# Kernel optimization log

Hardware: AMD Instinct MI355X
Metric: run time of the kernel (lower is better)

Reference implementation:

```python
import jax, jax.numpy as jnp
import numpy as np

BLOCK_SIZE = 32
QMAX = 31.0   # 6-bit symmetric: representable range [-32, 31], scale by absmax/31
QMIN = -32.0


def axs6_dequant(w: jnp.ndarray, block_size: int = BLOCK_SIZE) -> jnp.ndarray:
    """Block-wise 6-bit symmetric fake-quantization (quantize + dequantize)."""
    shape = w.shape
    wf = w.reshape(-1, block_size)                       # [n_blocks, block]
    scale = jnp.max(jnp.abs(wf), axis=1, keepdims=True) / QMAX
    scale = jnp.where(scale == 0, jnp.ones_like(scale), scale)
    q = jnp.clip(jnp.round(wf / scale), QMIN, QMAX)
    return (q * scale).reshape(shape)


def setup_inputs() -> dict:
    key = jax.random.key(0)
    k_x, k_w, k_b = jax.random.split(key, 3)
    C_in, C_out, K = 256, 512, 3
    x = jax.random.normal(k_x, (32, C_in, 56, 56), dtype=jnp.float32)
    # kaiming_uniform_(a=sqrt(5)) -> bound = sqrt(6 / ((1 + 5) * fan_in)) = 1/sqrt(fan_in)
    fan_in = C_in * K * K
    bound = 1.0 / np.sqrt(fan_in)
    weight = jax.random.uniform(k_w, (C_out, C_in, K, K), dtype=jnp.float32,
                                minval=-bound, maxval=bound)
    bias = jax.random.uniform(k_b, (C_out,), dtype=jnp.float32,
                              minval=-bound, maxval=bound)
    return {"x": x, "weight": weight, "bias": bias}


def reference(x, weight, bias):
    w_dq = axs6_dequant(weight, BLOCK_SIZE)
    out = jax.lax.conv_general_dilated(
        x, w_dq,
        window_strides=(1, 1),
        padding=((1, 1), (1, 1)),
        rhs_dilation=(1, 1),
        feature_group_count=1,
        dimension_numbers=("NCHW", "OIHW", "NCHW"),
    )
    return out + bias[None, :, None, None]
```

## Files before the change

kernel.cpp:

```cpp
#include <hip/hip_runtime.h>
#include <hip/hip_bf16.h>

typedef __bf16 bf16_t;
typedef __attribute__((ext_vector_type(8))) __bf16 bf16x8;
typedef __attribute__((ext_vector_type(4))) float f32x4;

#define C_IN   256
#define C_OUT  512
#define HW     3136
#define NB     32
#define HP     58
#define NQBLK  36864

#define BM   256
#define BN   224
#define BPIX 352
#define NWG  896

typedef const __attribute__((address_space(1))) unsigned int gu32;
typedef __attribute__((address_space(3))) unsigned int lu32;
__device__ __forceinline__ void gl16(const void* g, void* l) {
    __builtin_amdgcn_global_load_lds((gu32*)g, (lu32*)l, 16, 0, 0);
}
#define BAR()    __builtin_amdgcn_s_barrier()
#define PRIO(x)  __builtin_amdgcn_s_setprio(x)
#define SCHED0() __builtin_amdgcn_sched_barrier(0)

__global__ void k_dequant(const float* __restrict__ w, bf16_t* __restrict__ wt) {
    int b = blockIdx.x * blockDim.x + threadIdx.x;
    if (b >= NQBLK) return;
    const float* src = w + (size_t)b * 32;
    float v[32];
    float amax = 0.f;
    #pragma unroll
    for (int i = 0; i < 32; i += 4) {
        float4 t = *reinterpret_cast<const float4*>(src + i);
        v[i] = t.x; v[i+1] = t.y; v[i+2] = t.z; v[i+3] = t.w;
        amax = fmaxf(amax, fmaxf(fmaxf(fabsf(t.x), fabsf(t.y)),
                                 fmaxf(fabsf(t.z), fabsf(t.w))));
    }
    float scale = amax / 31.0f;
    if (scale == 0.f) scale = 1.f;
    #pragma unroll
    for (int i = 0; i < 32; i++) {
        float q = rintf(v[i] / scale);
        q = fminf(31.f, fmaxf(-32.f, q));
        float dq = q * scale;
        int flat = b * 32 + i;
        int p    = flat % 9;
        int rest = flat / 9;
        int ci   = rest & 255;
        int co   = rest >> 8;
        wt[((size_t)(p * C_OUT + co) << 8) + ci] = (bf16_t)dq;
    }
}

__global__ void k_halo_zero(bf16_t* __restrict__ xT) {
    int idx = blockIdx.x * 256 + threadIdx.x;
    if (idx >= NB * 228 * 32) return;
    int c8 = idx & 31;
    int t  = idx >> 5;
    int p  = t % 228;
    int n  = t / 228;
    int hh, ww;
    if      (p < 58)  { hh = 0;           ww = p; }
    else if (p < 116) { hh = 57;          ww = p - 58; }
    else if (p < 172) { hh = p - 116 + 1; ww = 0; }
    else              { hh = p - 172 + 1; ww = 57; }
    size_t e = (((size_t)n * HP + hh) * HP + ww) * C_IN + c8 * 8;
    *reinterpret_cast<uint4*>(xT + e) = make_uint4(0, 0, 0, 0);
}

__global__ void k_x_nhwc(const float* __restrict__ x, bf16_t* __restrict__ xT) {
    __shared__ float tile[64][65];
    const int n   = blockIdx.z;
    const int cb  = blockIdx.y * 64;
    const int hwb = blockIdx.x * 64;
    const int t   = threadIdx.x;

    const int col = t & 63;
    const int r0  = t >> 6;
    #pragma unroll
    for (int k = 0; k < 16; k++) {
        int r = r0 * 16 + k;
        tile[r][col] = x[((size_t)(n * C_IN + cb + r)) * HW + hwb + col];
    }
    __syncthreads();

    const int j  = t >> 2;
    const int co = (t & 3) * 16;
    const int hw = hwb + j;
    const int hh = hw / 56, ww = hw - hh * 56;
    __align__(16) bf16_t vals[16];
    #pragma unroll
    for (int k = 0; k < 16; k++)
        vals[k] = (bf16_t)tile[co + k][j];
    bf16_t* dst = xT + (((size_t)n * HP + hh + 1) * HP + (ww + 1)) * C_IN + cb + co;
    *reinterpret_cast<uint4*>(dst)     = *reinterpret_cast<uint4*>(&vals[0]);
    *reinterpret_cast<uint4*>(dst + 8) = *reinterpret_cast<uint4*>(&vals[8]);
}

__global__ __launch_bounds__(512, 2) void k_conv_gemm(
    const bf16_t* __restrict__ xT, const bf16_t* __restrict__ wt,
    const float* __restrict__ bias, float* __restrict__ out)
{
    __shared__ __align__(16) bf16_t As[2][BM][64];
    __shared__ __align__(16) bf16_t Bs[2][BPIX][64];

    const int tid  = threadIdx.x;
    const int lane = tid & 63;
    const int wid  = tid >> 6;
    const int wr   = wid >> 1;
    const int wc   = wid & 1;

    const int orig  = blockIdx.x;
    const int wgid  = (orig & 7) * 112 + (orig >> 3);
    const int co0   = (wgid & 1) * BM;
    const int sband = wgid >> 1;
    const int nimg  = sband / 14;
    const int R0    = (sband - nimg * 14) * 4;

    const int prow = tid >> 3;
    const int lcx  = (tid & 7) ^ (prow & 7);

    const bf16_t* pAsrc = wt + ((size_t)(co0 + prow) << 8) + lcx * 8;
    const bf16_t* pBsrc = xT + ((size_t)(nimg * HP + R0) * HP + prow) * C_IN + lcx * 8;

    auto stageA = [&](int buf, int c, int p) {
        const bf16_t* src = pAsrc + ((size_t)p << 17) + (c << 6);
        bf16_t* dst = &As[buf][wid * 8][0];
        #pragma unroll
        for (int i = 0; i < 4; i++)
            gl16(src + (i << 14), dst + i * 4096);
    };
    auto stageB = [&](int buf, int c) {
        const bf16_t* src = pBsrc + (c << 6);
        bf16_t* dst = &Bs[buf][wid * 8][0];
        #pragma unroll
        for (int i = 0; i < 5; i++)
            gl16(src + i * 16384, dst + i * 4096);
        if (tid < 224)
            gl16(src + 5 * 16384, dst + 5 * 4096);
    };

    const int rl = lane & 15;
    const int kg = lane >> 4;

    int a_off[4][2];
    #pragma unroll
    for (int m = 0; m < 4; m++) {
        int row = wr * 64 + m * 16 + rl;
        a_off[m][0] = row * 64 + ((kg       ^ (rl & 7)) * 8);
        a_off[m][1] = row * 64 + (((4 + kg) ^ (rl & 7)) * 8);
    }
    int base_pix[7];
    #pragma unroll
    for (int j = 0; j < 7; j++) {
        int nn = wc * 112 + j * 16 + rl;
        int br = nn / 56, bc = nn - br * 56;
        base_pix[j] = (br + 1) * 58 + bc + 1;
    }

    f32x4 acc[4][7];
    #pragma unroll
    for (int m = 0; m < 4; m++)
        #pragma unroll
        for (int j = 0; j < 7; j++)
            acc[m][j] = f32x4{0.f, 0.f, 0.f, 0.f};

    stageB(0, 0);
    stageA(0, 0, 0);
    asm volatile("s_waitcnt vmcnt(0)" ::: "memory");
    BAR();
    SCHED0();

    bf16x8 aF[4][2], bF[7][2];

    #pragma unroll 1
    for (int c = 0; c < 4; ++c) {
        const int cb = c & 1;
        #pragma unroll 1
        for (int p = 0; p < 9; ++p) {
            const int t    = c * 9 + p;
            const int tpar = t & 1;

            if (t + 1 < 36) {
                int pn = (p == 8) ? 0 : p + 1;
                int cn = (p == 8) ? c + 1 : c;
                stageA(tpar ^ 1, cn, pn);
            }
            if (p == 1 && c < 3)
                stageB(cb ^ 1, c + 1);

            const int q3 = p / 3;
            const int sh = (q3 - 1) * 58 + (p - q3 * 3) - 1;

            const bf16_t* abase = &As[tpar][0][0];
            #pragma unroll
            for (int m = 0; m < 4; m++) {
                aF[m][0] = *reinterpret_cast<const bf16x8*>(abase + a_off[m][0]);
                aF[m][1] = *reinterpret_cast<const bf16x8*>(abase + a_off[m][1]);
            }
            const bf16_t* bbase = &Bs[cb][0][0];
            #pragma unroll
            for (int j = 0; j < 7; j++) {
                int pix = base_pix[j] + sh;
                const bf16_t* rp = bbase + pix * 64;
                int key = (pix & 7);
                bF[j][0] = *reinterpret_cast<const bf16x8*>(rp + ((kg       ^ key) * 8));
                bF[j][1] = *reinterpret_cast<const bf16x8*>(rp + (((4 + kg) ^ key) * 8));
            }

            PRIO(1);
            #pragma unroll
            for (int m = 0; m < 4; m++)
                #pragma unroll
                for (int j = 0; j < 7; j++) {
                    acc[m][j] = __builtin_amdgcn_mfma_f32_16x16x32_bf16(aF[m][0], bF[j][0], acc[m][j], 0, 0, 0);
                    acc[m][j] = __builtin_amdgcn_mfma_f32_16x16x32_bf16(aF[m][1], bF[j][1], acc[m][j], 0, 0, 0);
                }
            PRIO(0);

            asm volatile("s_waitcnt vmcnt(0)" ::: "memory");
            BAR();
            SCHED0();
        }
    }

    int hw_off[7];
    #pragma unroll
    for (int j = 0; j < 7; j++) {
        int nn = wc * 112 + j * 16 + rl;
        int br = nn / 56, bc = nn - br * 56;
        hw_off[j] = (R0 + br) * 56 + bc;
    }
    const size_t obase = (size_t)nimg * C_OUT * HW;
    #pragma unroll
    for (int m = 0; m < 4; m++) {
        int cob = co0 + wr * 64 + m * 16 + ((lane >> 4) << 2);
        #pragma unroll
        for (int i = 0; i < 4; i++) {
            int co = cob + i;
            float bv = bias[co];
            float* orow = out + obase + (size_t)co * HW;
            #pragma unroll
            for (int j = 0; j < 7; j++)
                orow[hw_off[j]] = acc[m][j][i] + bv;
        }
    }
}

extern "C" void kernel_launch(void* const* d_in, const int* in_sizes, int n_in,
                              void* d_out, int out_size, void* d_ws, size_t ws_size,
                              hipStream_t stream) {
    const float* x    = (const float*)d_in[0];
    const float* w    = (const float*)d_in[1];
    const float* bias = (const float*)d_in[2];
    float* out = (float*)d_out;

    bf16_t* xT = (bf16_t*)d_ws;
    bf16_t* wt = (bf16_t*)((char*)d_ws + (size_t)NB * HP * HP * C_IN * 2);

    k_halo_zero<<<dim3((NB * 228 * 32 + 255) / 256), dim3(256), 0, stream>>>(xT);
    k_x_nhwc<<<dim3(49, 4, NB), dim3(256), 0, stream>>>(x, xT);
    k_dequant<<<dim3((NQBLK + 255) / 256), dim3(256), 0, stream>>>(w, wt);
    k_conv_gemm<<<dim3(NWG), dim3(512), 0, stream>>>(xT, wt, bias, out);
}
```

Before: 314.7 us.

## Halve K-tile to 32 and add a triple-buffered A pipeline with split B staging

Shrinks the per-step reduction chunk from 64 to 32 channels, which halves LDS per buffer and doubles the number of main-loop iterations. The weight tile becomes triple-buffered with a two-step prefetch, and the waitcnt is relaxed to vmcnt(2) so one load stays in flight across the barrier. The input-band staging is split into three parts spread over iterations. The aim is to overlap global loads with MFMA work and raise occupancy, at the cost of twice as many barriers and a smaller MFMA batch per barrier.

```diff
diff --git a/kernel.cpp b/kernel.cpp
--- a/kernel.cpp
+++ b/kernel.cpp
@@ -12,9 +12,7 @@
 #define HP     58
 #define NQBLK  36864
 
-#define BM   256
-#define BN   224
-#define BPIX 352
+#define BK   32
 #define NWG  896
 
 typedef const __attribute__((address_space(1))) unsigned int gu32;
@@ -104,8 +102,8 @@
     const bf16_t* __restrict__ xT, const bf16_t* __restrict__ wt,
     const float* __restrict__ bias, float* __restrict__ out)
 {
-    __shared__ __align__(16) bf16_t As[2][BM][64];
-    __shared__ __align__(16) bf16_t Bs[2][BPIX][64];
+    __shared__ __align__(16) bf16_t As[3][256][BK];
+    __shared__ __align__(16) bf16_t Bs[2][384][BK];
 
     const int tid  = threadIdx.x;
     const int lane = tid & 63;
@@ -115,50 +113,43 @@
 
     const int orig  = blockIdx.x;
     const int wgid  = (orig & 7) * 112 + (orig >> 3);
-    const int co0   = (wgid & 1) * BM;
+    const int co0   = (wgid & 1) * 256;
     const int sband = wgid >> 1;
     const int nimg  = sband / 14;
     const int R0    = (sband - nimg * 14) * 4;
 
-    const int prow = tid >> 3;
-    const int lcx  = (tid & 7) ^ (prow & 7);
-
-    const bf16_t* pAsrc = wt + ((size_t)(co0 + prow) << 8) + lcx * 8;
-    const bf16_t* pBsrc = xT + ((size_t)(nimg * HP + R0) * HP + prow) * C_IN + lcx * 8;
-
-    auto stageA = [&](int buf, int c, int p) {
-        const bf16_t* src = pAsrc + ((size_t)p << 17) + (c << 6);
-        bf16_t* dst = &As[buf][wid * 8][0];
-        #pragma unroll
-        for (int i = 0; i < 4; i++)
-            gl16(src + (i << 14), dst + i * 4096);
+    const int trow = tid >> 2;
+    const int lcx  = (tid & 3) ^ ((trow ^ (trow >> 2)) & 3);
+    const bf16_t* pAsrc = wt + ((size_t)(co0 + trow) << 8) + lcx * 8;
+    const size_t bandStart = (size_t)(nimg * HP + R0) * HP;
+    const bf16_t* pBsrc = xT + (bandStart + trow) * C_IN + lcx * 8;
+
+    auto stageA = [&](int slot, int cn, int pn) {
+        const bf16_t* src = pAsrc + ((size_t)pn << 17) + (cn << 5);
+        bf16_t* dst = &As[slot][0][0] + wid * 512;
+        gl16(src, dst);
+        gl16(src + (128 << 8), dst + 4096);
     };
-    auto stageB = [&](int buf, int c) {
-        const bf16_t* src = pBsrc + (c << 6);
-        bf16_t* dst = &Bs[buf][wid * 8][0];
-        #pragma unroll
-        for (int i = 0; i < 5; i++)
-            gl16(src + i * 16384, dst + i * 4096);
-        if (tid < 224)
-            gl16(src + 5 * 16384, dst + 5 * 4096);
+    auto stageBpart = [&](int buf, int cn, int part) {
+        const bf16_t* src = pBsrc + ((size_t)part << 15) + (cn << 5);
+        bf16_t* dst = &Bs[buf][0][0] + part * 4096 + wid * 512;
+        gl16(src, dst);
     };
 
     const int rl = lane & 15;
     const int kg = lane >> 4;
-
-    int a_off[4][2];
+    int a_off[4];
     #pragma unroll
     for (int m = 0; m < 4; m++) {
         int row = wr * 64 + m * 16 + rl;
-        a_off[m][0] = row * 64 + ((kg       ^ (rl & 7)) * 8);
-        a_off[m][1] = row * 64 + (((4 + kg) ^ (rl & 7)) * 8);
-    }
-    int base_pix[7];
+        a_off[m] = row * BK + ((kg ^ ((row ^ (row >> 2)) & 3)) * 8);
+    }
+    int bpix[7];
     #pragma unroll
     for (int j = 0; j < 7; j++) {
         int nn = wc * 112 + j * 16 + rl;
         int br = nn / 56, bc = nn - br * 56;
-        base_pix[j] = (br + 1) * 58 + bc + 1;
+        bpix[j] = (br + 1) * 58 + bc + 1;
     }
 
     f32x4 acc[4][7];
@@ -168,62 +159,61 @@
         for (int j = 0; j < 7; j++)
             acc[m][j] = f32x4{0.f, 0.f, 0.f, 0.f};
 
-    stageB(0, 0);
+    stageBpart(0, 0, 0); stageBpart(0, 0, 1); stageBpart(0, 0, 2);
     stageA(0, 0, 0);
-    asm volatile("s_waitcnt vmcnt(0)" ::: "memory");
+    stageA(1, 0, 1);
+    asm volatile("s_waitcnt vmcnt(2)" ::: "memory");
     BAR();
     SCHED0();
 
-    bf16x8 aF[4][2], bF[7][2];
+    bf16x8 aF[4], bF[7];
+    int sr = 0;
 
     #pragma unroll 1
-    for (int c = 0; c < 4; ++c) {
-        const int cb = c & 1;
+    for (int c = 0; c < 8; ++c) {
+        const int bb = c & 1;
         #pragma unroll 1
         for (int p = 0; p < 9; ++p) {
-            const int t    = c * 9 + p;
-            const int tpar = t & 1;
-
-            if (t + 1 < 36) {
-                int pn = (p == 8) ? 0 : p + 1;
-                int cn = (p == 8) ? c + 1 : c;
-                stageA(tpar ^ 1, cn, pn);
+            const int t = c * 9 + p;
+
+            if (t < 70) {
+                int pn = p + 2, cn = c;
+                if (pn >= 9) { pn -= 9; cn++; }
+                int sw = sr + 2; if (sw >= 3) sw -= 3;
+                stageA(sw, cn, pn);
             }
-            if (p == 1 && c < 3)
-                stageB(cb ^ 1, c + 1);
+            if (c < 7 && p >= 1 && p <= 3)
+                stageBpart(bb ^ 1, c + 1, p - 1);
 
             const int q3 = p / 3;
             const int sh = (q3 - 1) * 58 + (p - q3 * 3) - 1;
-
-            const bf16_t* abase = &As[tpar][0][0];
-            #pragma unroll
-            for (int m = 0; m < 4; m++) {
-                aF[m][0] = *reinterpret_cast<const bf16x8*>(abase + a_off[m][0]);
-                aF[m][1] = *reinterpret_cast<const bf16x8*>(abase + a_off[m][1]);
-            }
-            const bf16_t* bbase = &Bs[cb][0][0];
+            const bf16_t* ab = &As[sr][0][0];
+            #pragma unroll
+            for (int m = 0; m < 4; m++)
+                aF[m] = *reinterpret_cast<const bf16x8*>(ab + a_off[m]);
+            const bf16_t* bbp = &Bs[bb][0][0];
             #pragma unroll
             for (int j = 0; j < 7; j++) {
-                int pix = base_pix[j] + sh;
-                const bf16_t* rp = bbase + pix * 64;
-                int key = (pix & 7);
-                bF[j][0] = *reinterpret_cast<const bf16x8*>(rp + ((kg       ^ key) * 8));
-                bF[j][1] = *reinterpret_cast<const bf16x8*>(rp + (((4 + kg) ^ key) * 8));
+                int pix = bpix[j] + sh;
+                int off = pix * BK + ((kg ^ ((pix ^ (pix >> 2)) & 3)) * 8);
+                bF[j] = *reinterpret_cast<const bf16x8*>(bbp + off);
             }
 
             PRIO(1);
             #pragma unroll
             for (int m = 0; m < 4; m++)
                 #pragma unroll
-                for (int j = 0; j < 7; j++) {
-                    acc[m][j] = __builtin_amdgcn_mfma_f32_16x16x32_bf16(aF[m][0], bF[j][0], acc[m][j], 0, 0, 0);
-                    acc[m][j] = __builtin_amdgcn_mfma_f32_16x16x32_bf16(aF[m][1], bF[j][1], acc[m][j], 0, 0, 0);
-                }
+                for (int j = 0; j < 7; j++)
+                    acc[m][j] = __builtin_amdgcn_mfma_f32_16x16x32_bf16(aF[m], bF[j], acc[m][j], 0, 0, 0);
             PRIO(0);
 
-            asm volatile("s_waitcnt vmcnt(0)" ::: "memory");
+            if (t < 70)
+                asm volatile("s_waitcnt vmcnt(2)" ::: "memory");
+            else
+                asm volatile("s_waitcnt vmcnt(0)" ::: "memory");
             BAR();
             SCHED0();
+            sr++; if (sr >= 3) sr -= 3;
         }
     }
 
```

Measured after the change: 361.2 us. +14.8%, slower.

## Stage shifted input tiles per tap and split K-step into four barrier-interleaved phases

Applied to the files above, without the earlier changes.

Replaces the halo-band input tile, which was loaded once per channel chunk and indexed with per-tap pixel shifts, with a per-tap B tile of 224 shifted pixels reloaded every K-step. Each K-step is split into four phases so B and A global-to-LDS loads for the next steps are issued between MFMA groups. A is prefetched two steps ahead and B one step ahead. This aims to overlap loads with MFMA work and shrink LDS footprint, but it reloads input data nine times per channel chunk and adds many more barriers per step.

```diff
diff --git a/kernel.cpp b/kernel.cpp
--- a/kernel.cpp
+++ b/kernel.cpp
@@ -12,9 +12,7 @@
 #define HP     58
 #define NQBLK  36864
 
-#define BM   256
-#define BN   224
-#define BPIX 352
+#define NT   36
 #define NWG  896
 
 typedef const __attribute__((address_space(1))) unsigned int gu32;
@@ -104,8 +102,8 @@
     const bf16_t* __restrict__ xT, const bf16_t* __restrict__ wt,
     const float* __restrict__ bias, float* __restrict__ out)
 {
-    __shared__ __align__(16) bf16_t As[2][BM][64];
-    __shared__ __align__(16) bf16_t Bs[2][BPIX][64];
+    __shared__ __align__(16) bf16_t As[2][256][64];
+    __shared__ __align__(16) bf16_t Bs[2][224][64];
 
     const int tid  = threadIdx.x;
     const int lane = tid & 63;
@@ -115,50 +113,60 @@
 
     const int orig  = blockIdx.x;
     const int wgid  = (orig & 7) * 112 + (orig >> 3);
-    const int co0   = (wgid & 1) * BM;
+    const int co0   = (wgid & 1) * 256;
     const int sband = wgid >> 1;
     const int nimg  = sband / 14;
     const int R0    = (sband - nimg * 14) * 4;
 
-    const int prow = tid >> 3;
-    const int lcx  = (tid & 7) ^ (prow & 7);
-
-    const bf16_t* pAsrc = wt + ((size_t)(co0 + prow) << 8) + lcx * 8;
-    const bf16_t* pBsrc = xT + ((size_t)(nimg * HP + R0) * HP + prow) * C_IN + lcx * 8;
-
-    auto stageA = [&](int buf, int c, int p) {
-        const bf16_t* src = pAsrc + ((size_t)p << 17) + (c << 6);
-        bf16_t* dst = &As[buf][wid * 8][0];
+    const int trow = tid >> 3;
+    const int lcx  = (tid & 7) ^ (trow & 7);
+
+    const bf16_t* pA[4];
+    const bf16_t* pB[4];
+    #pragma unroll
+    for (int i = 0; i < 4; i++) {
+        pA[i] = wt + ((size_t)(co0 + i * 64 + trow) << 8) + lcx * 8;
+        int r  = i * 64 + trow;
+        int br = r / 56, bc = r - br * 56;
+        pB[i] = xT + (((size_t)nimg * HP + R0 + br + 1) * HP + (bc + 1)) * C_IN + lcx * 8;
+    }
+
+    auto stageA = [&](int buf, int tk) {
+        const size_t off = ((size_t)(tk >> 2) << 17) + ((tk & 3) << 6);
+        bf16_t* dst = &As[buf][0][0] + wid * 512;
         #pragma unroll
         for (int i = 0; i < 4; i++)
-            gl16(src + (i << 14), dst + i * 4096);
+            gl16(pA[i] + off, dst + i * 4096);
     };
-    auto stageB = [&](int buf, int c) {
-        const bf16_t* src = pBsrc + (c << 6);
-        bf16_t* dst = &Bs[buf][wid * 8][0];
-        #pragma unroll
-        for (int i = 0; i < 5; i++)
-            gl16(src + i * 16384, dst + i * 4096);
-        if (tid < 224)
-            gl16(src + 5 * 16384, dst + 5 * 4096);
+    auto stageB = [&](int buf, int tk, int half) {
+        const int p  = tk >> 2;
+        const int q3 = p / 3;
+        const int off = ((q3 - 1) * HP + (p - q3 * 3) - 1) * C_IN + ((tk & 3) << 6);
+        bf16_t* dst = &Bs[buf][0][0] + wid * 512;
+        if (half == 0) {
+            gl16(pB[0] + off, dst);
+            gl16(pB[1] + off, dst + 4096);
+        } else {
+            gl16(pB[2] + off, dst + 8192);
+            if (tid < 256)
+                gl16(pB[3] + off, dst + 12288);
+        }
     };
 
     const int rl = lane & 15;
     const int kg = lane >> 4;
-
-    int a_off[4][2];
+    int a_off[4][2], b_off[7][2];
     #pragma unroll
     for (int m = 0; m < 4; m++) {
         int row = wr * 64 + m * 16 + rl;
-        a_off[m][0] = row * 64 + ((kg       ^ (rl & 7)) * 8);
-        a_off[m][1] = row * 64 + (((4 + kg) ^ (rl & 7)) * 8);
-    }
-    int base_pix[7];
+        a_off[m][0] = row * 64 + ((kg       ^ (row & 7)) * 8);
+        a_off[m][1] = row * 64 + (((4 + kg) ^ (row & 7)) * 8);
+    }
     #pragma unroll
     for (int j = 0; j < 7; j++) {
-        int nn = wc * 112 + j * 16 + rl;
-        int br = nn / 56, bc = nn - br * 56;
-        base_pix[j] = (br + 1) * 58 + bc + 1;
+        int row = wc * 112 + j * 16 + rl;
+        b_off[j][0] = row * 64 + ((kg       ^ (row & 7)) * 8);
+        b_off[j][1] = row * 64 + (((4 + kg) ^ (row & 7)) * 8);
     }
 
     f32x4 acc[4][7];
@@ -168,63 +176,104 @@
         for (int j = 0; j < 7; j++)
             acc[m][j] = f32x4{0.f, 0.f, 0.f, 0.f};
 
-    stageB(0, 0);
-    stageA(0, 0, 0);
-    asm volatile("s_waitcnt vmcnt(0)" ::: "memory");
+    stageA(0, 0);
+    stageB(0, 0, 0); stageB(0, 0, 1);
+    stageA(1, 1);
+    asm volatile("s_waitcnt vmcnt(4)" ::: "memory");
     BAR();
     SCHED0();
 
-    bf16x8 aF[4][2], bF[7][2];
+    bf16x8 aF[4][2], bF[2][2];
 
     #pragma unroll 1
-    for (int c = 0; c < 4; ++c) {
-        const int cb = c & 1;
-        #pragma unroll 1
-        for (int p = 0; p < 9; ++p) {
-            const int t    = c * 9 + p;
-            const int tpar = t & 1;
-
-            if (t + 1 < 36) {
-                int pn = (p == 8) ? 0 : p + 1;
-                int cn = (p == 8) ? c + 1 : c;
-                stageA(tpar ^ 1, cn, pn);
+    for (int t = 0; t < NT; ++t) {
+        const int cur = t & 1;
+        const bf16_t* ab = &As[cur][0][0];
+        const bf16_t* bb = &Bs[cur][0][0];
+
+        #pragma unroll
+        for (int m = 0; m < 4; m++) {
+            aF[m][0] = *reinterpret_cast<const bf16x8*>(ab + a_off[m][0]);
+            aF[m][1] = *reinterpret_cast<const bf16x8*>(ab + a_off[m][1]);
+        }
+        #pragma unroll
+        for (int j = 0; j < 2; j++) {
+            bF[j][0] = *reinterpret_cast<const bf16x8*>(bb + b_off[j][0]);
+            bF[j][1] = *reinterpret_cast<const bf16x8*>(bb + b_off[j][1]);
+        }
+        if (t + 1 < NT) stageB(cur ^ 1, t + 1, 0);
+        BAR();
+        asm volatile("s_waitcnt lgkmcnt(0)" ::: "memory");
+        SCHED0();
+        PRIO(1);
+        #pragma unroll
+        for (int m = 0; m < 4; m++)
+            #pragma unroll
+            for (int j = 0; j < 2; j++) {
+                acc[m][j] = __builtin_amdgcn_mfma_f32_16x16x32_bf16(aF[m][0], bF[j][0], acc[m][j], 0, 0, 0);
+                acc[m][j] = __builtin_amdgcn_mfma_f32_16x16x32_bf16(aF[m][1], bF[j][1], acc[m][j], 0, 0, 0);
             }
-            if (p == 1 && c < 3)
-                stageB(cb ^ 1, c + 1);
-
-            const int q3 = p / 3;
-            const int sh = (q3 - 1) * 58 + (p - q3 * 3) - 1;
-
-            const bf16_t* abase = &As[tpar][0][0];
+        PRIO(0);
+        BAR();
+
+        #pragma unroll
+        for (int j = 0; j < 2; j++) {
+            bF[j][0] = *reinterpret_cast<const bf16x8*>(bb + b_off[j + 2][0]);
+            bF[j][1] = *reinterpret_cast<const bf16x8*>(bb + b_off[j + 2][1]);
+        }
+        if (t + 1 < NT) stageB(cur ^ 1, t + 1, 1);
+        BAR();
+        asm volatile("s_waitcnt lgkmcnt(0)" ::: "memory");
+        SCHED0();
+        PRIO(1);
+        #pragma unroll
+        for (int m = 0; m < 4; m++)
             #pragma unroll
-            for (int m = 0; m < 4; m++) {
-                aF[m][0] = *reinterpret_cast<const bf16x8*>(abase + a_off[m][0]);
-                aF[m][1] = *reinterpret_cast<const bf16x8*>(abase + a_off[m][1]);
+            for (int j = 0; j < 2; j++) {
+                acc[m][j + 2] = __builtin_amdgcn_mfma_f32_16x16x32_bf16(aF[m][0], bF[j][0], acc[m][j + 2], 0, 0, 0);
+                acc[m][j + 2] = __builtin_amdgcn_mfma_f32_16x16x32_bf16(aF[m][1], bF[j][1], acc[m][j + 2], 0, 0, 0);
             }
-            const bf16_t* bbase = &Bs[cb][0][0];
+        PRIO(0);
+        BAR();
+
+        #pragma unroll
+        for (int j = 0; j < 2; j++) {
+            bF[j][0] = *reinterpret_cast<const bf16x8*>(bb + b_off[j + 4][0]);
+            bF[j][1] = *reinterpret_cast<const bf16x8*>(bb + b_off[j + 4][1]);
+        }
+        BAR();
+        asm volatile("s_waitcnt lgkmcnt(0)" ::: "memory");
+        SCHED0();
+        PRIO(1);
+        #pragma unroll
+        for (int m = 0; m < 4; m++)
             #pragma unroll
-            for (int j = 0; j < 7; j++) {
-                int pix = base_pix[j] + sh;
-                const bf16_t* rp = bbase + pix * 64;
-                int key = (pix & 7);
-                bF[j][0] = *reinterpret_cast<const bf16x8*>(rp + ((kg       ^ key) * 8));
-                bF[j][1] = *reinterpret_cast<const bf16x8*>(rp + (((4 + kg) ^ key) * 8));
+            for (int j = 0; j < 2; j++) {
+                acc[m][j + 4] = __builtin_amdgcn_mfma_f32_16x16x32_bf16(aF[m][0], bF[j][0], acc[m][j + 4], 0, 0, 0);
+                acc[m][j + 4] = __builtin_amdgcn_mfma_f32_16x16x32_bf16(aF[m][1], bF[j][1], acc[m][j + 4], 0, 0, 0);
             }
-
-            PRIO(1);
-            #pragma unroll
-            for (int m = 0; m < 4; m++)
-                #pragma unroll
-                for (int j = 0; j < 7; j++) {
-                    acc[m][j] = __builtin_amdgcn_mfma_f32_16x16x32_bf16(aF[m][0], bF[j][0], acc[m][j], 0, 0, 0);
-                    acc[m][j] = __builtin_amdgcn_mfma_f32_16x16x32_bf16(aF[m][1], bF[j][1], acc[m][j], 0, 0, 0);
-                }
-            PRIO(0);
-
+        PRIO(0);
+        BAR();
+
+        bF[0][0] = *reinterpret_cast<const bf16x8*>(bb + b_off[6][0]);
+        bF[0][1] = *reinterpret_cast<const bf16x8*>(bb + b_off[6][1]);
+        if (t + 2 < NT) stageA(cur, t + 2);
+        BAR();
+        asm volatile("s_waitcnt lgkmcnt(0)" ::: "memory");
+        SCHED0();
+        PRIO(1);
+        #pragma unroll
+        for (int m = 0; m < 4; m++) {
+            acc[m][6] = __builtin_amdgcn_mfma_f32_16x16x32_bf16(aF[m][0], bF[0][0], acc[m][6], 0, 0, 0);
+            acc[m][6] = __builtin_amdgcn_mfma_f32_16x16x32_bf16(aF[m][1], bF[0][1], acc[m][6], 0, 0, 0);
+        }
+        PRIO(0);
+        if (t + 2 < NT)
+            asm volatile("s_waitcnt vmcnt(4)" ::: "memory");
+        else
             asm volatile("s_waitcnt vmcnt(0)" ::: "memory");
-            BAR();
-            SCHED0();
-        }
+        BAR();
+        SCHED0();
     }
 
     int hw_off[7];
```

After: 316.3 us. No clear change (+0.5%).

## Replace band-tiled conv GEMM with smaller 128x128 implicit-GEMM tiles

Applied to the files above, without the earlier changes.

The conv GEMM moves from 512-thread workgroups with 256-channel by 4-row spatial bands, where the input band is staged once per channel chunk and reused across all nine taps, to 256-thread workgroups computing 128x128 tiles over flattened pixels. Each of the 36 K-steps now restages both the weight tile and a shifted input tile. This drops the per-tap input reuse from the halo band and adds global traffic. In exchange it gets more workgroups, higher occupancy per CU and simpler, uniform staging.

```diff
diff --git a/kernel.cpp b/kernel.cpp
--- a/kernel.cpp
+++ b/kernel.cpp
@@ -12,10 +12,8 @@
 #define HP     58
 #define NQBLK  36864
 
-#define BM   256
-#define BN   224
-#define BPIX 352
-#define NWG  896
+#define NT   36
+#define NWG  3136
 
 typedef const __attribute__((address_space(1))) unsigned int gu32;
 typedef __attribute__((address_space(3))) unsigned int lu32;
@@ -100,12 +98,12 @@
     *reinterpret_cast<uint4*>(dst + 8) = *reinterpret_cast<uint4*>(&vals[8]);
 }
 
-__global__ __launch_bounds__(512, 2) void k_conv_gemm(
+__global__ __launch_bounds__(256, 4) void k_conv_gemm(
     const bf16_t* __restrict__ xT, const bf16_t* __restrict__ wt,
     const float* __restrict__ bias, float* __restrict__ out)
 {
-    __shared__ __align__(16) bf16_t As[2][BM][64];
-    __shared__ __align__(16) bf16_t Bs[2][BPIX][64];
+    __shared__ __align__(16) bf16_t As[2][128][64];
+    __shared__ __align__(16) bf16_t Bs[2][128][64];
 
     const int tid  = threadIdx.x;
     const int lane = tid & 63;
@@ -113,128 +111,122 @@
     const int wr   = wid >> 1;
     const int wc   = wid & 1;
 
-    const int orig  = blockIdx.x;
-    const int wgid  = (orig & 7) * 112 + (orig >> 3);
-    const int co0   = (wgid & 1) * BM;
-    const int sband = wgid >> 1;
-    const int nimg  = sband / 14;
-    const int R0    = (sband - nimg * 14) * 4;
-
-    const int prow = tid >> 3;
-    const int lcx  = (tid & 7) ^ (prow & 7);
-
-    const bf16_t* pAsrc = wt + ((size_t)(co0 + prow) << 8) + lcx * 8;
-    const bf16_t* pBsrc = xT + ((size_t)(nimg * HP + R0) * HP + prow) * C_IN + lcx * 8;
-
-    auto stageA = [&](int buf, int c, int p) {
-        const bf16_t* src = pAsrc + ((size_t)p << 17) + (c << 6);
-        bf16_t* dst = &As[buf][wid * 8][0];
+    const int orig = blockIdx.x;
+    const int wgid = (orig & 7) * 392 + (orig >> 3);
+    const int co0  = (wgid & 3) * 128;
+    const int s0   = (wgid >> 2) * 128;
+
+    const int trow = tid >> 3;
+    const int lcx  = (tid & 7) ^ (trow & 7);
+
+    int aoff[4], boff[4];
+    #pragma unroll
+    for (int i = 0; i < 4; i++) {
+        aoff[i] = ((co0 + i * 32 + trow) << 8) + lcx * 8;
+        int px = s0 + i * 32 + trow;
+        int n  = px / HW;
+        int hw = px - n * HW;
+        int hh = hw / 56, ww = hw - hh * 56;
+        boff[i] = ((n * HP + hh + 1) * HP + ww + 1) * C_IN + lcx * 8;
+    }
+
+    auto stage = [&](int buf, int tk) {
+        const int p  = tk >> 2;
+        const int kc = (tk & 3) << 6;
+        const size_t aT = (size_t)p * (C_OUT << 8) + kc;
+        const int q3 = p / 3;
+        const int bT = ((q3 - 1) * HP + (p - q3 * 3) - 1) * C_IN + kc;
+        bf16_t* dA = &As[buf][0][0] + wid * 512;
+        bf16_t* dB = &Bs[buf][0][0] + wid * 512;
         #pragma unroll
         for (int i = 0; i < 4; i++)
-            gl16(src + (i << 14), dst + i * 4096);
-    };
-    auto stageB = [&](int buf, int c) {
-        const bf16_t* src = pBsrc + (c << 6);
-        bf16_t* dst = &Bs[buf][wid * 8][0];
-        #pragma unroll
-        for (int i = 0; i < 5; i++)
-            gl16(src + i * 16384, dst + i * 4096);
-        if (tid < 224)
-            gl16(src + 5 * 16384, dst + 5 * 4096);
+            gl16(wt + aoff[i] + aT, dA + i * 2048);
+        #pragma unroll
+        for (int i = 0; i < 4; i++)
+            gl16(xT + boff[i] + bT, dB + i * 2048);
     };
 
     const int rl = lane & 15;
     const int kg = lane >> 4;
-
-    int a_off[4][2];
+    int a_off[4][2], b_off[4][2];
     #pragma unroll
     for (int m = 0; m < 4; m++) {
         int row = wr * 64 + m * 16 + rl;
         a_off[m][0] = row * 64 + ((kg       ^ (rl & 7)) * 8);
         a_off[m][1] = row * 64 + (((4 + kg) ^ (rl & 7)) * 8);
     }
-    int base_pix[7];
-    #pragma unroll
-    for (int j = 0; j < 7; j++) {
-        int nn = wc * 112 + j * 16 + rl;
-        int br = nn / 56, bc = nn - br * 56;
-        base_pix[j] = (br + 1) * 58 + bc + 1;
-    }
-
-    f32x4 acc[4][7];
+    #pragma unroll
+    for (int j = 0; j < 4; j++) {
+        int row = wc * 64 + j * 16 + rl;
+        b_off[j][0] = row * 64 + ((kg       ^ (rl & 7)) * 8);
+        b_off[j][1] = row * 64 + (((4 + kg) ^ (rl & 7)) * 8);
+    }
+
+    f32x4 acc[4][4];
     #pragma unroll
     for (int m = 0; m < 4; m++)
         #pragma unroll
-        for (int j = 0; j < 7; j++)
+        for (int j = 0; j < 4; j++)
             acc[m][j] = f32x4{0.f, 0.f, 0.f, 0.f};
 
-    stageB(0, 0);
-    stageA(0, 0, 0);
+    stage(0, 0);
     asm volatile("s_waitcnt vmcnt(0)" ::: "memory");
     BAR();
     SCHED0();
 
-    bf16x8 aF[4][2], bF[7][2];
-
     #pragma unroll 1
-    for (int c = 0; c < 4; ++c) {
-        const int cb = c & 1;
-        #pragma unroll 1
-        for (int p = 0; p < 9; ++p) {
-            const int t    = c * 9 + p;
-            const int tpar = t & 1;
-
-            if (t + 1 < 36) {
-                int pn = (p == 8) ? 0 : p + 1;
-                int cn = (p == 8) ? c + 1 : c;
-                stageA(tpar ^ 1, cn, pn);
-            }
-            if (p == 1 && c < 3)
-                stageB(cb ^ 1, c + 1);
-
-            const int q3 = p / 3;
-            const int sh = (q3 - 1) * 58 + (p - q3 * 3) - 1;
-
-            const bf16_t* abase = &As[tpar][0][0];
-            #pragma unroll
-            for (int m = 0; m < 4; m++) {
-                aF[m][0] = *reinterpret_cast<const bf16x8*>(abase + a_off[m][0]);
-                aF[m][1] = *reinterpret_cast<const bf16x8*>(abase + a_off[m][1]);
-            }
-            const bf16_t* bbase = &Bs[cb][0][0];
-            #pragma unroll
-            for (int j = 0; j < 7; j++) {
-                int pix = base_pix[j] + sh;
-                const bf16_t* rp = bbase + pix * 64;
-                int key = (pix & 7);
-                bF[j][0] = *reinterpret_cast<const bf16x8*>(rp + ((kg       ^ key) * 8));
-                bF[j][1] = *reinterpret_cast<const bf16x8*>(rp + (((4 + kg) ^ key) * 8));
-            }
-
+    for (int t = 0; t < NT; ++t) {
+        const int cur = t & 1;
+        if (t + 1 < NT) stage(cur ^ 1, t + 1);
+
+        const bf16_t* ab = &As[cur][0][0];
+        const bf16_t* bb = &Bs[cur][0][0];
+
+        {
+            bf16x8 aF[4], bF[4];
+            #pragma unroll
+            for (int m = 0; m < 4; m++)
+                aF[m] = *reinterpret_cast<const bf16x8*>(ab + a_off[m][0]);
+            #pragma unroll
+            for (int j = 0; j < 4; j++)
+                bF[j] = *reinterpret_cast<const bf16x8*>(bb + b_off[j][0]);
             PRIO(1);
             #pragma unroll
             for (int m = 0; m < 4; m++)
                 #pragma unroll
-                for (int j = 0; j < 7; j++) {
-                    acc[m][j] = __builtin_amdgcn_mfma_f32_16x16x32_bf16(aF[m][0], bF[j][0], acc[m][j], 0, 0, 0);
-                    acc[m][j] = __builtin_amdgcn_mfma_f32_16x16x32_bf16(aF[m][1], bF[j][1], acc[m][j], 0, 0, 0);
-                }
+                for (int j = 0; j < 4; j++)
+                    acc[m][j] = __builtin_amdgcn_mfma_f32_16x16x32_bf16(aF[m], bF[j], acc[m][j], 0, 0, 0);
             PRIO(0);
-
-            asm volatile("s_waitcnt vmcnt(0)" ::: "memory");
-            BAR();
-            SCHED0();
         }
-    }
-
-    int hw_off[7];
-    #pragma unroll
-    for (int j = 0; j < 7; j++) {
-        int nn = wc * 112 + j * 16 + rl;
-        int br = nn / 56, bc = nn - br * 56;
-        hw_off[j] = (R0 + br) * 56 + bc;
-    }
-    const size_t obase = (size_t)nimg * C_OUT * HW;
+        {
+            bf16x8 aF[4], bF[4];
+            #pragma unroll
+            for (int m = 0; m < 4; m++)
+                aF[m] = *reinterpret_cast<const bf16x8*>(ab + a_off[m][1]);
+            #pragma unroll
+            for (int j = 0; j < 4; j++)
+                bF[j] = *reinterpret_cast<const bf16x8*>(bb + b_off[j][1]);
+            PRIO(1);
+            #pragma unroll
+            for (int m = 0; m < 4; m++)
+                #pragma unroll
+                for (int j = 0; j < 4; j++)
+                    acc[m][j] = __builtin_amdgcn_mfma_f32_16x16x32_bf16(aF[m], bF[j], acc[m][j], 0, 0, 0);
+            PRIO(0);
+        }
+
+        asm volatile("s_waitcnt vmcnt(0)" ::: "memory");
+        BAR();
+        SCHED0();
+    }
+
+    int pxn[4], pxhw[4];
+    #pragma unroll
+    for (int j = 0; j < 4; j++) {
+        int px = s0 + wc * 64 + j * 16 + rl;
+        pxn[j]  = px / HW;
+        pxhw[j] = px - pxn[j] * HW;
+    }
     #pragma unroll
     for (int m = 0; m < 4; m++) {
         int cob = co0 + wr * 64 + m * 16 + ((lane >> 4) << 2);
@@ -242,10 +234,9 @@
         for (int i = 0; i < 4; i++) {
             int co = cob + i;
             float bv = bias[co];
-            float* orow = out + obase + (size_t)co * HW;
-            #pragma unroll
-            for (int j = 0; j < 7; j++)
-                orow[hw_off[j]] = acc[m][j][i] + bv;
+            #pragma unroll
+            for (int j = 0; j < 4; j++)
+                out[((size_t)(pxn[j] * C_OUT + co)) * HW + pxhw[j]] = acc[m][j][i] + bv;
         }
     }
 }
@@ -264,5 +255,5 @@
     k_halo_zero<<<dim3((NB * 228 * 32 + 255) / 256), dim3(256), 0, stream>>>(xT);
     k_x_nhwc<<<dim3(49, 4, NB), dim3(256), 0, stream>>>(x, xT);
     k_dequant<<<dim3((NQBLK + 255) / 256), dim3(256), 0, stream>>>(w, wt);
-    k_conv_gemm<<<dim3(NWG), dim3(512), 0, stream>>>(xT, wt, bias, out);
-}
+    k_conv_gemm<<<dim3(NWG), dim3(256), 0, stream>>>(xT, wt, bias, out);
+}
```

Result: no change. 312.7 us (-0.7%).
